# Kernel tuning notes

Hardware: AMD Instinct MI355X
Metric: run time of the kernel (lower is better)

## Reference

```python
import jax, jax.numpy as jnp
import numpy as np

B, N, D, H = 8, 1024, 768, 12
HD = D // H  # 64


def setup_inputs() -> dict:
    key = jax.random.key(0)
    ks = jax.random.split(key, 10)
    input_graph = jax.random.normal(ks[0], (B, N, D), dtype=jnp.float32)
    u = jax.random.uniform(ks[1], (B, N, N), dtype=jnp.float32)
    keep = jax.random.uniform(ks[2], (B, N, N)) < 0.15
    adj = jnp.where(keep, u, 0.0)
    s = 1.0 / np.sqrt(D)
    Wq = jax.random.normal(ks[3], (D, D), dtype=jnp.float32) * s
    bq = jnp.zeros((D,), dtype=jnp.float32)
    Wk = jax.random.normal(ks[4], (D, D), dtype=jnp.float32) * s
    bk = jnp.zeros((D,), dtype=jnp.float32)
    Wv = jax.random.normal(ks[5], (D, D), dtype=jnp.float32) * s
    bv = jnp.zeros((D,), dtype=jnp.float32)
    beta = jnp.asarray(0.1, dtype=jnp.float32)
    return {"input_graph": input_graph, "adj": adj, "Wq": Wq, "bq": bq,
            "Wk": Wk, "bk": bk, "Wv": Wv, "bv": bv, "beta": beta}


def _split_heads(x):
    # [B,N,D] -> [B,H,N,HD]
    b, n, _ = x.shape
    return x.reshape(b, n, H, HD).transpose(0, 2, 1, 3)


def reference(input_graph, adj, Wq, bq, Wk, bk, Wv, bv, beta):
    q = _split_heads(input_graph @ Wq + bq)  # [B,H,N,HD]
    k = _split_heads(input_graph @ Wk + bk)
    v = _split_heads(input_graph @ Wv + bv)
    scores = jnp.einsum('bhqd,bhkd->bhqk', q, k) / jnp.sqrt(jnp.asarray(HD, input_graph.dtype))
    adj_e = adj[:, None, :, :]  # [B,1,N,N]
    scores = scores + beta * adj_e
    scores = jnp.where(adj_e > 0, scores, jnp.asarray(-9e15, scores.dtype))
    probs = jax.nn.softmax(scores, axis=-1)
    out = jnp.einsum('bhqk,bhkd->bhqd', probs, v)  # [B,H,N,HD]
    return out.transpose(0, 2, 1, 3).reshape(input_graph.shape[0], input_graph.shape[1], D)
```

## Files before the change

### kernel.cpp

```cpp
#include <hip/hip_runtime.h>

#define B_ 8
#define N_ 1024
#define D_ 768
#define H_ 12
#define HD_ 64

#define LOG2E 1.4426950408889634f

typedef __attribute__((ext_vector_type(8))) short bf16x8;
typedef __attribute__((ext_vector_type(4))) short short4_t;
typedef __attribute__((ext_vector_type(4))) float f32x4;
typedef __attribute__((ext_vector_type(2))) unsigned int u32x2;
typedef unsigned int u32;

__device__ __forceinline__ short f2bf(float f) {
  union { float f; unsigned u; } v; v.f = f;
  unsigned u = v.u;
  unsigned r = u + 0x7fffu + ((u >> 16) & 1u);
  return (short)(r >> 16);
}
__device__ __forceinline__ float bf2f(short s) {
  union { unsigned u; float f; } v;
  v.u = ((unsigned)(unsigned short)s) << 16;
  return v.f;
}
__device__ __forceinline__ float bpermf(int srclane, float x) {
  union { float f; int i; } v; v.f = x;
  union { int i; float f; } r;
  r.i = __builtin_amdgcn_ds_bpermute(srclane * 4, v.i);
  return r.f;
}
__device__ __forceinline__ float max3f(float a, float b, float c) {
  return fmaxf(fmaxf(a, b), c);
}
__device__ __forceinline__ u32 cvtpk(float a, float b) {
  u32 r;
  asm("v_cvt_pk_bf16_f32 %0, %1, %2" : "=v"(r) : "v"(a), "v"(b));
  return r;
}

__device__ __forceinline__ void gload_lds16(const void* g, void* l) {
  __builtin_amdgcn_global_load_lds((const __attribute__((address_space(1))) u32*)g,
                                   (__attribute__((address_space(3))) u32*)l, 16, 0, 0);
}

__global__ void cvt_x_kernel(const float* __restrict__ X, short* __restrict__ Xb) {
  int i = (blockIdx.x * 256 + threadIdx.x) * 8;
  float4 a = *(const float4*)(X + i);
  float4 b = *(const float4*)(X + i + 4);
  bf16x8 o;
  o[0] = f2bf(a.x); o[1] = f2bf(a.y); o[2] = f2bf(a.z); o[3] = f2bf(a.w);
  o[4] = f2bf(b.x); o[5] = f2bf(b.y); o[6] = f2bf(b.z); o[7] = f2bf(b.w);
  *(bf16x8*)(Xb + i) = o;
}

__global__ void cvt_w_kernel(const float* __restrict__ Wq, const float* __restrict__ Wk,
                             const float* __restrict__ Wv, short* __restrict__ Wt3) {
  const float* W = blockIdx.z == 0 ? Wq : (blockIdx.z == 1 ? Wk : Wv);
  short* O = Wt3 + (size_t)blockIdx.z * D_ * D_;
  __shared__ float t[32][33];
  int n0 = blockIdx.x * 32, k0 = blockIdx.y * 32;
  int tx = threadIdx.x, ty = threadIdx.y;
#pragma unroll
  for (int j = 0; j < 4; j++)
    t[ty + 8 * j][tx] = W[(size_t)(k0 + ty + 8 * j) * D_ + n0 + tx];
  __syncthreads();
#pragma unroll
  for (int j = 0; j < 4; j++)
    O[(size_t)(n0 + ty + 8 * j) * D_ + k0 + tx] = f2bf(t[tx][ty + 8 * j]);
}

__global__ __launch_bounds__(256)
void madj_kernel(const float* __restrict__ adj, const float* __restrict__ beta_p,
                 short* __restrict__ madjF) {
  const int qt = blockIdx.x, kt = blockIdx.y, b = blockIdx.z;
  const int tid = threadIdx.x;
  const float b2 = beta_p[0] * LOG2E;
  const float MASKV = -9.0e15f * LOG2E;

  __shared__ float Lt[64][68];
  {
    const int row = tid >> 2, cs = (tid & 3) * 16;
    const float* ap = adj + ((size_t)b * N_ + qt * 64 + row) * (size_t)N_ + kt * 64 + cs;
#pragma unroll
    for (int j = 0; j < 4; j++)
      *(float4*)&Lt[row][cs + 4 * j] = *(const float4*)(ap + 4 * j);
  }
  __syncthreads();

  const int lane = tid & 63, w = tid >> 6;
  const int l15 = lane & 15, lg = lane >> 4;
  const int q = 16 * w + l15;
  short vals[16];
#pragma unroll
  for (int cb = 0; cb < 4; cb++) {
    float4 a4 = *(const float4*)&Lt[q][16 * cb + 4 * lg];
    float av[4] = {a4.x, a4.y, a4.z, a4.w};
#pragma unroll
    for (int r = 0; r < 4; r++) {
      float a = av[r];
      vals[cb * 4 + r] = f2bf((a > 0.f) ? b2 * a : MASKV);
    }
  }
  short* o = madjF + (((size_t)(b * 16 + qt) * 16 + kt) * 256 + tid) * 16;
  bf16x8 lo, hi;
#pragma unroll
  for (int j = 0; j < 8; j++) { lo[j] = vals[j]; hi[j] = vals[8 + j]; }
  *(bf16x8*)o = lo;
  *(bf16x8*)(o + 8) = hi;
}

__global__ __launch_bounds__(256, 4)
void qkv_gemm_kernel(const short* __restrict__ Xb, const short* __restrict__ Wt3,
                     const float* __restrict__ bq, const float* __restrict__ bk,
                     const float* __restrict__ bv, short* __restrict__ QKV) {
  const int z = blockIdx.z;
  const short* Wt = Wt3 + (size_t)z * D_ * D_;
  const float* bias = z == 0 ? bq : (z == 1 ? bk : bv);
  short* C = QKV + (size_t)z * (B_ * N_) * D_;
  const float alpha = (z == 0) ? 0.125f * LOG2E : 1.0f;

  const int m0 = blockIdx.x * 128;
  const int n0 = blockIdx.y * 128;
  const int tid = threadIdx.x;
  const int lane = tid & 63;
  const int wid = tid >> 6;
  const int wr = (wid >> 1) * 64;
  const int wc = (wid & 1) * 64;
  const int l15 = lane & 15;
  const int lg = lane >> 4;

  __shared__ short At[2][128][32];
  __shared__ short Bt[2][128][32];

  f32x4 acc[4][4];
#pragma unroll
  for (int m = 0; m < 4; m++)
#pragma unroll
    for (int n = 0; n < 4; n++)
      acc[m][n] = (f32x4){0.f, 0.f, 0.f, 0.f};

  const int srow_l = lane >> 2;
  const int sc8 = (((lane & 3) ^ ((lane >> 2) & 3)) * 8);
  const short* ag = Xb + (size_t)(m0 + wid * 16 + srow_l) * D_ + sc8;
  const short* bg = Wt + (size_t)(n0 + wid * 16 + srow_l) * D_ + sc8;

  auto stage = [&](int bi, int k0) {
#pragma unroll
    for (int p = 0; p < 2; p++) {
      gload_lds16(ag + (size_t)(64 * p) * D_ + k0,
                  ((short*)At[bi]) + (size_t)(wid + 4 * p) * 512);
      gload_lds16(bg + (size_t)(64 * p) * D_ + k0,
                  ((short*)Bt[bi]) + (size_t)(wid + 4 * p) * 512);
    }
  };

  stage(0, 0);
  for (int k0 = 0; k0 < D_; k0 += 32) {
    const int cur = (k0 >> 5) & 1;
    __syncthreads();
    if (k0 + 32 < D_) stage(cur ^ 1, k0 + 32);

    bf16x8 af[4], bfr[4];
#pragma unroll
    for (int m = 0; m < 4; m++) {
      const int row = wr + m * 16 + l15;
      af[m] = *(const bf16x8*)&At[cur][row][(lg ^ (l15 & 3)) * 8];
    }
#pragma unroll
    for (int n = 0; n < 4; n++) {
      const int row = wc + n * 16 + l15;
      bfr[n] = *(const bf16x8*)&Bt[cur][row][(lg ^ (l15 & 3)) * 8];
    }
#pragma unroll
    for (int m = 0; m < 4; m++)
#pragma unroll
      for (int n = 0; n < 4; n++)
        acc[m][n] = __builtin_amdgcn_mfma_f32_16x16x32_bf16(af[m], bfr[n], acc[m][n], 0, 0, 0);
  }

  if (z == 2) {
#pragma unroll
    for (int n = 0; n < 4; n++) {
      const int col = n0 + wc + n * 16 + l15;
      const float bval = bias[col];
      const int hh = col >> 6, dd = col & 63;
#pragma unroll
      for (int m = 0; m < 4; m++) {
        const int row = m0 + wr + m * 16 + 4 * lg;
        const int bb = row >> 10, nn = row & 1023;
        short4_t o;
#pragma unroll
        for (int r = 0; r < 4; r++) o[r] = f2bf(acc[m][n][r] + bval);
        *(short4_t*)&C[(((size_t)bb * H_ + hh) * HD_ + dd) * N_ + nn] = o;
      }
    }
  } else {
#pragma unroll
    for (int n = 0; n < 4; n++) {
      const int col = n0 + wc + n * 16 + l15;
      const float bval = bias[col];
#pragma unroll
      for (int m = 0; m < 4; m++) {
#pragma unroll
        for (int r = 0; r < 4; r++) {
          const int row = m0 + wr + m * 16 + 4 * lg + r;
          C[(size_t)row * D_ + col] = f2bf((acc[m][n][r] + bval) * alpha);
        }
      }
    }
  }
}

__global__ __launch_bounds__(512, 4)
void attn_kernel(const short* __restrict__ QKV, const short* __restrict__ madjF,
                 float* __restrict__ out) {
  const short* Qb = QKV;
  const short* Kb = QKV + (size_t)(B_ * N_) * D_;
  const short* VTg = QKV + 2 * (size_t)(B_ * N_) * D_;

  const int wg = blockIdx.x;
  const int b = wg & 7;
  const int rem = wg >> 3;
  const int h = rem >> 3;
  const int qt = rem & 7;

  const int tid = threadIdx.x;
  const int lane = tid & 63;
  const int w = tid >> 6;
  const int l15 = lane & 15;
  const int lg = lane >> 4;

  const int q0 = qt * 128;
  const size_t seq0 = (size_t)b * N_;
  const int hc = h * HD_;

  __shared__ short Kt[2][64][64];
  __shared__ short VTt[2][64][64];
  __shared__ short Pt[8][16][64];

  bf16x8 qf[2];
  {
    const short* qp = Qb + (seq0 + q0 + 16 * w + l15) * (size_t)D_ + hc + 8 * lg;
    qf[0] = *(const bf16x8*)qp;
    qf[1] = *(const bf16x8*)(qp + 32);
  }

  f32x4 acc[4];
#pragma unroll
  for (int cb = 0; cb < 4; cb++) acc[cb] = (f32x4){0.f, 0.f, 0.f, 0.f};
  float m_ = -__builtin_inff();
  float l_ = 0.f;

  const int srow = 8 * w + (lane >> 3);
  const int sc8 = ((lane & 7) ^ (lane >> 3)) * 8;
  const short* kg = Kb + (seq0 + srow) * (size_t)D_ + hc + sc8;
  const short* vg = VTg + ((size_t)(b * H_ + h) * HD_ + srow) * N_ + sc8;
  const int qm = 2 * qt + (w >> 2);
  const short* mg = madjF + ((size_t)(b * 16 + qm) * 16) * 4096 + ((w & 3) * 64 + lane) * 16;

  const int sw2 = (l15 & 7) << 1;
  char* ptrow = (char*)&Pt[w][l15][0];

  auto stage = [&](int bi, int kt) {
    const int k0 = kt * 64;
    gload_lds16(kg + (size_t)k0 * D_, ((short*)Kt[bi]) + (size_t)w * 512);
    gload_lds16(vg + k0, ((short*)VTt[bi]) + (size_t)w * 512);
  };

  stage(0, 0);
  bf16x8 mlo = *(const bf16x8*)mg;
  bf16x8 mhi = *(const bf16x8*)(mg + 8);

  for (int kt = 0; kt < 16; kt++) {
    const int cur = kt & 1;
    __syncthreads();
    if (kt < 15) stage(cur ^ 1, kt + 1);
    const int ktn = kt < 15 ? kt + 1 : 15;
    bf16x8 mlo2 = *(const bf16x8*)(mg + (size_t)ktn * 4096);
    bf16x8 mhi2 = *(const bf16x8*)(mg + (size_t)ktn * 4096 + 8);

    f32x4 s[4];
#pragma unroll
    for (int cb = 0; cb < 4; cb++) {
      f32x4 c;
#pragma unroll
      for (int r = 0; r < 4; r++)
        c[r] = bf2f(cb < 2 ? mlo[(cb & 1) * 4 + r] : mhi[(cb & 1) * 4 + r]);
      const int swk = l15 & 7;
      bf16x8 kf0 = *(const bf16x8*)&Kt[cur][cb * 16 + l15][(lg ^ swk) * 8];
      bf16x8 kf1 = *(const bf16x8*)&Kt[cur][cb * 16 + l15][((lg + 4) ^ swk) * 8];
      c = __builtin_amdgcn_mfma_f32_16x16x32_bf16(kf0, qf[0], c, 0, 0, 0);
      s[cb] = __builtin_amdgcn_mfma_f32_16x16x32_bf16(kf1, qf[1], c, 0, 0, 0);
    }
    mlo = mlo2; mhi = mhi2;

    float tm = max3f(max3f(s[0][0], s[0][1], s[0][2]),
                     max3f(s[0][3], s[1][0], s[1][1]),
                     max3f(s[1][2], s[1][3], s[2][0]));
    float tm2 = max3f(max3f(s[2][1], s[2][2], s[2][3]),
                      max3f(s[3][0], s[3][1], s[3][2]), s[3][3]);
    tm = fmaxf(tm, tm2);
    tm = fmaxf(tm, __shfl_xor(tm, 16));
    tm = fmaxf(tm, __shfl_xor(tm, 32));

    if (!__all(tm <= m_ + 8.f)) {
      const float mnew = fmaxf(m_, tm);
      const float sc2 = __builtin_exp2f(m_ - mnew);
      m_ = mnew;
      l_ *= sc2;
      float scr[4];
#pragma unroll
      for (int r = 0; r < 4; r++) scr[r] = bpermf(4 * lg + r, sc2);
#pragma unroll
      for (int cb = 0; cb < 4; cb++)
#pragma unroll
        for (int r = 0; r < 4; r++) acc[cb][r] *= scr[r];
    }

    float ps = 0.f;
    u32 pk[8];
#pragma unroll
    for (int cb = 0; cb < 4; cb++) {
#pragma unroll
      for (int rp = 0; rp < 2; rp++) {
        const float p0 = __builtin_exp2f(s[cb][2 * rp] - m_);
        const float p1 = __builtin_exp2f(s[cb][2 * rp + 1] - m_);
        ps += p0 + p1;
        pk[cb * 2 + rp] = cvtpk(p0, p1);
      }
    }
    ps += __shfl_xor(ps, 16);
    ps += __shfl_xor(ps, 32);
    l_ += ps;

#pragma unroll
    for (int cb = 0; cb < 4; cb++) {
      u32x2 wv = {pk[2 * cb], pk[2 * cb + 1]};
      *(u32x2*)(ptrow + (((4 * cb + lg) ^ sw2) << 3)) = wv;
    }

#pragma unroll
    for (int ks = 0; ks < 2; ks++) {
      bf16x8 pa = *(const bf16x8*)(ptrow + ((((lg << 1) + 8 * ks) ^ sw2) << 3));
#pragma unroll
      for (int cb = 0; cb < 4; cb++) {
        const int row = cb * 16 + l15;
        bf16x8 vb = *(const bf16x8*)&VTt[cur][row][((lg + 4 * ks) ^ (row & 7)) * 8];
        acc[cb] = __builtin_amdgcn_mfma_f32_16x16x32_bf16(pa, vb, acc[cb], 0, 0, 0);
      }
    }
  }

  float inv[4];
#pragma unroll
  for (int r = 0; r < 4; r++) inv[r] = 1.f / bpermf(4 * lg + r, l_);
#pragma unroll
  for (int cb = 0; cb < 4; cb++) {
#pragma unroll
    for (int r = 0; r < 4; r++) {
      out[(seq0 + q0 + 16 * w + 4 * lg + r) * (size_t)D_ + hc + cb * 16 + l15] =
          acc[cb][r] * inv[r];
    }
  }
}

extern "C" void kernel_launch(void* const* d_in, const int* in_sizes, int n_in,
                              void* d_out, int out_size, void* d_ws, size_t ws_size,
                              hipStream_t stream) {
  const float* X    = (const float*)d_in[0];
  const float* adj  = (const float*)d_in[1];
  const float* Wq   = (const float*)d_in[2];
  const float* bq   = (const float*)d_in[3];
  const float* Wk   = (const float*)d_in[4];
  const float* bk   = (const float*)d_in[5];
  const float* Wv   = (const float*)d_in[6];
  const float* bv   = (const float*)d_in[7];
  const float* beta = (const float*)d_in[8];
  float* out = (float*)d_out;

  short* Xb    = (short*)d_ws;
  short* Wt3   = Xb + (size_t)(B_ * N_) * D_;
  short* QKV   = Wt3 + 3 * (size_t)D_ * D_;
  short* madjF = QKV + 3 * (size_t)(B_ * N_) * D_;

  cvt_x_kernel<<<dim3((B_ * N_ * D_) / (256 * 8)), 256, 0, stream>>>(X, Xb);
  cvt_w_kernel<<<dim3(24, 24, 3), dim3(32, 8), 0, stream>>>(Wq, Wk, Wv, Wt3);
  madj_kernel<<<dim3(16, 16, 8), 256, 0, stream>>>(adj, beta, madjF);
  qkv_gemm_kernel<<<dim3(64, 6, 3), 256, 0, stream>>>(Xb, Wt3, bq, bk, bv, QKV);
  attn_kernel<<<dim3(768), 512, 0, stream>>>(QKV, madjF, out);
}
```

Baseline: 127.1 us.

## Fuse adjacency masking into attention kernel and add MFMA priority hints

Removes the separate kernel that precomputed a bf16 masked/scaled adjacency tile layout. The attention kernel now loads fp32 adj directly, prefetching the next tile into registers, and computes the mask and beta scaling inline as the MFMA accumulator seed. This saves a launch and the write/read of the intermediate buffer, but every head now reads fp32 adj (twice the bytes per head) with a less contiguous access pattern. It also wraps the MFMA sections in s_setprio to favour matrix issue across waves.

```diff
diff --git a/kernel.cpp b/kernel.cpp
--- a/kernel.cpp
+++ b/kernel.cpp
@@ -19,11 +19,6 @@
   unsigned u = v.u;
   unsigned r = u + 0x7fffu + ((u >> 16) & 1u);
   return (short)(r >> 16);
-}
-__device__ __forceinline__ float bf2f(short s) {
-  union { unsigned u; float f; } v;
-  v.u = ((unsigned)(unsigned short)s) << 16;
-  return v.f;
 }
 __device__ __forceinline__ float bpermf(int srclane, float x) {
   union { float f; int i; } v; v.f = x;
@@ -69,46 +64,6 @@
 #pragma unroll
   for (int j = 0; j < 4; j++)
     O[(size_t)(n0 + ty + 8 * j) * D_ + k0 + tx] = f2bf(t[tx][ty + 8 * j]);
-}
-
-__global__ __launch_bounds__(256)
-void madj_kernel(const float* __restrict__ adj, const float* __restrict__ beta_p,
-                 short* __restrict__ madjF) {
-  const int qt = blockIdx.x, kt = blockIdx.y, b = blockIdx.z;
-  const int tid = threadIdx.x;
-  const float b2 = beta_p[0] * LOG2E;
-  const float MASKV = -9.0e15f * LOG2E;
-
-  __shared__ float Lt[64][68];
-  {
-    const int row = tid >> 2, cs = (tid & 3) * 16;
-    const float* ap = adj + ((size_t)b * N_ + qt * 64 + row) * (size_t)N_ + kt * 64 + cs;
-#pragma unroll
-    for (int j = 0; j < 4; j++)
-      *(float4*)&Lt[row][cs + 4 * j] = *(const float4*)(ap + 4 * j);
-  }
-  __syncthreads();
-
-  const int lane = tid & 63, w = tid >> 6;
-  const int l15 = lane & 15, lg = lane >> 4;
-  const int q = 16 * w + l15;
-  short vals[16];
-#pragma unroll
-  for (int cb = 0; cb < 4; cb++) {
-    float4 a4 = *(const float4*)&Lt[q][16 * cb + 4 * lg];
-    float av[4] = {a4.x, a4.y, a4.z, a4.w};
-#pragma unroll
-    for (int r = 0; r < 4; r++) {
-      float a = av[r];
-      vals[cb * 4 + r] = f2bf((a > 0.f) ? b2 * a : MASKV);
-    }
-  }
-  short* o = madjF + (((size_t)(b * 16 + qt) * 16 + kt) * 256 + tid) * 16;
-  bf16x8 lo, hi;
-#pragma unroll
-  for (int j = 0; j < 8; j++) { lo[j] = vals[j]; hi[j] = vals[8 + j]; }
-  *(bf16x8*)o = lo;
-  *(bf16x8*)(o + 8) = hi;
 }
 
 __global__ __launch_bounds__(256, 4)
@@ -214,8 +169,8 @@
 }
 
 __global__ __launch_bounds__(512, 4)
-void attn_kernel(const short* __restrict__ QKV, const short* __restrict__ madjF,
-                 float* __restrict__ out) {
+void attn_kernel(const short* __restrict__ QKV, const float* __restrict__ adj,
+                 const float* __restrict__ beta_p, float* __restrict__ out) {
   const short* Qb = QKV;
   const short* Kb = QKV + (size_t)(B_ * N_) * D_;
   const short* VTg = QKV + 2 * (size_t)(B_ * N_) * D_;
@@ -235,6 +190,8 @@
   const int q0 = qt * 128;
   const size_t seq0 = (size_t)b * N_;
   const int hc = h * HD_;
+  const float b2 = beta_p[0] * LOG2E;
+  const float MASKV = -9.0e15f * LOG2E;
 
   __shared__ short Kt[2][64][64];
   __shared__ short VTt[2][64][64];
@@ -257,8 +214,7 @@
   const int sc8 = ((lane & 7) ^ (lane >> 3)) * 8;
   const short* kg = Kb + (seq0 + srow) * (size_t)D_ + hc + sc8;
   const short* vg = VTg + ((size_t)(b * H_ + h) * HD_ + srow) * N_ + sc8;
-  const int qm = 2 * qt + (w >> 2);
-  const short* mg = madjF + ((size_t)(b * 16 + qm) * 16) * 4096 + ((w & 3) * 64 + lane) * 16;
+  const float* ar = adj + ((size_t)b * N_ + q0 + 16 * w + l15) * (size_t)N_ + 4 * lg;
 
   const int sw2 = (l15 & 7) << 1;
   char* ptrow = (char*)&Pt[w][l15][0];
@@ -270,31 +226,40 @@
   };
 
   stage(0, 0);
-  bf16x8 mlo = *(const bf16x8*)mg;
-  bf16x8 mhi = *(const bf16x8*)(mg + 8);
+  f32x4 avn[4];
+#pragma unroll
+  for (int cb = 0; cb < 4; cb++) avn[cb] = *(const f32x4*)(ar + cb * 16);
 
   for (int kt = 0; kt < 16; kt++) {
     const int cur = kt & 1;
     __syncthreads();
     if (kt < 15) stage(cur ^ 1, kt + 1);
-    const int ktn = kt < 15 ? kt + 1 : 15;
-    bf16x8 mlo2 = *(const bf16x8*)(mg + (size_t)ktn * 4096);
-    bf16x8 mhi2 = *(const bf16x8*)(mg + (size_t)ktn * 4096 + 8);
+    f32x4 av[4];
+#pragma unroll
+    for (int cb = 0; cb < 4; cb++) av[cb] = avn[cb];
+    if (kt < 15) {
+#pragma unroll
+      for (int cb = 0; cb < 4; cb++)
+        avn[cb] = *(const f32x4*)(ar + (kt + 1) * 64 + cb * 16);
+    }
 
     f32x4 s[4];
+    __builtin_amdgcn_s_setprio(1);
 #pragma unroll
     for (int cb = 0; cb < 4; cb++) {
       f32x4 c;
 #pragma unroll
-      for (int r = 0; r < 4; r++)
-        c[r] = bf2f(cb < 2 ? mlo[(cb & 1) * 4 + r] : mhi[(cb & 1) * 4 + r]);
+      for (int r = 0; r < 4; r++) {
+        const float a = av[cb][r];
+        c[r] = (a > 0.f) ? a * b2 : MASKV;
+      }
       const int swk = l15 & 7;
       bf16x8 kf0 = *(const bf16x8*)&Kt[cur][cb * 16 + l15][(lg ^ swk) * 8];
       bf16x8 kf1 = *(const bf16x8*)&Kt[cur][cb * 16 + l15][((lg + 4) ^ swk) * 8];
       c = __builtin_amdgcn_mfma_f32_16x16x32_bf16(kf0, qf[0], c, 0, 0, 0);
       s[cb] = __builtin_amdgcn_mfma_f32_16x16x32_bf16(kf1, qf[1], c, 0, 0, 0);
     }
-    mlo = mlo2; mhi = mhi2;
+    __builtin_amdgcn_s_setprio(0);
 
     float tm = max3f(max3f(s[0][0], s[0][1], s[0][2]),
                      max3f(s[0][3], s[1][0], s[1][1]),
@@ -341,6 +306,7 @@
       *(u32x2*)(ptrow + (((4 * cb + lg) ^ sw2) << 3)) = wv;
     }
 
+    __builtin_amdgcn_s_setprio(1);
 #pragma unroll
     for (int ks = 0; ks < 2; ks++) {
       bf16x8 pa = *(const bf16x8*)(ptrow + ((((lg << 1) + 8 * ks) ^ sw2) << 3));
@@ -351,6 +317,7 @@
         acc[cb] = __builtin_amdgcn_mfma_f32_16x16x32_bf16(pa, vb, acc[cb], 0, 0, 0);
       }
     }
+    __builtin_amdgcn_s_setprio(0);
   }
 
   float inv[4];
@@ -383,11 +350,9 @@
   short* Xb    = (short*)d_ws;
   short* Wt3   = Xb + (size_t)(B_ * N_) * D_;
   short* QKV   = Wt3 + 3 * (size_t)D_ * D_;
-  short* madjF = QKV + 3 * (size_t)(B_ * N_) * D_;
 
   cvt_x_kernel<<<dim3((B_ * N_ * D_) / (256 * 8)), 256, 0, stream>>>(X, Xb);
   cvt_w_kernel<<<dim3(24, 24, 3), dim3(32, 8), 0, stream>>>(Wq, Wk, Wv, Wt3);
-  madj_kernel<<<dim3(16, 16, 8), 256, 0, stream>>>(adj, beta, madjF);
   qkv_gemm_kernel<<<dim3(64, 6, 3), 256, 0, stream>>>(Xb, Wt3, bq, bk, bv, QKV);
-  attn_kernel<<<dim3(768), 512, 0, stream>>>(QKV, madjF, out);
-}
+  attn_kernel<<<dim3(768), 512, 0, stream>>>(QKV, adj, beta, out);
+}
```

Measured after the change: 148.6 us. 1.17x slower.
